# Kernel optimization log

Measured on AMD Instinct MI355X. Metric: run time of the kernel, lower is better.

## Reference

```python
import jax, jax.numpy as jnp
import numpy as np

C = 256        # branch_in_channels / head_conv
H, W = 160, 400
KPT_THR = 0.4  # forward_test default kpt_thr
ROOT_THR = 1.0 # self.root_thr
EPS = 1e-4


def _conv(x, w, b):
    # NCHW conv, SAME padding
    y = jax.lax.conv_general_dilated(x, w, (1, 1), 'SAME',
                                     dimension_numbers=('NCHW', 'OIHW', 'NCHW'))
    return y + b[None, :, None, None]


def _ctnet_head(x, w1, b1, w2, b2):
    # CtnetHead: Conv3x3 -> ReLU -> Conv1x1
    return _conv(jax.nn.relu(_conv(x, w1, b1)), w2, b2)


def setup_inputs() -> dict:
    key = jax.random.key(0)
    ks = jax.random.split(key, 16)
    s = 0.02
    def w3(k, co, ci):
        return jax.random.normal(k, (co, ci, 3, 3), jnp.float32) * s
    def w1k(k, co, ci):
        return jax.random.normal(k, (co, ci, 1, 1), jnp.float32) * s
    inp = {'f_hm': jax.random.normal(ks[0], (1, C, H, W), jnp.float32)}
    # four heads: centerpts (hm:1), keypts (hm:1), offset (2ch), reg (2ch)
    names = [('cpt', 1), ('kpt', 1), ('off', 2), ('reg', 2)]
    i = 1
    for name, cout in names:
        inp[f'{name}_w1'] = w3(ks[i], C, C); i += 1
        inp[f'{name}_b1'] = jnp.zeros((C,), jnp.float32)
        inp[f'{name}_w2'] = w1k(ks[i], cout, C); i += 1
        inp[f'{name}_b2'] = jnp.zeros((cout,), jnp.float32)
    return inp


def reference(f_hm, cpt_w1, cpt_b1, cpt_w2, cpt_b2,
              kpt_w1, kpt_b1, kpt_w2, kpt_b2,
              off_w1, off_b1, off_w2, off_b2,
              reg_w1, reg_b1, reg_w2, reg_b2):
    # heads
    hm = jnp.clip(jax.nn.sigmoid(_ctnet_head(f_hm, cpt_w1, cpt_b1, cpt_w2, cpt_b2)), EPS, 1.0 - EPS)
    kpts_hm = jnp.clip(jax.nn.sigmoid(_ctnet_head(f_hm, kpt_w1, kpt_b1, kpt_w2, kpt_b2)), EPS, 1.0 - EPS)
    pts_offset = _ctnet_head(f_hm, off_w1, off_b1, off_w2, off_b2)   # [1,2,H,W]
    int_offset = _ctnet_head(f_hm, reg_w1, reg_b1, reg_w2, reg_b2)   # [1,2,H,W]

    # ktdet_decode_fast: (1,3) max-pool NMS along width
    hmax = jax.lax.reduce_window(kpts_hm, -jnp.inf, jax.lax.max,
                                 (1, 1, 1, 3), (1, 1, 1, 1),
                                 ((0, 0), (0, 0), (0, 0), (1, 1)))
    heat_nms = kpts_hm * (hmax == kpts_hm).astype(kpts_hm.dtype)    # [1,1,H,W]

    # root-center mask: offset_y < root_thr AND heat_nms > kpt_thr, transposed to [W,H]
    mask_low = ((pts_offset[0, 1] < ROOT_THR) & (heat_nms[0, 0] > KPT_THR)).T  # [W,H] bool

    # coordinate maps: coord_mat channels are (x, y), permuted to [H,W,2]
    xs = jnp.arange(W, dtype=jnp.float32)
    ys = jnp.arange(H, dtype=jnp.float32)
    coord = jnp.stack(jnp.meshgrid(xs, ys, indexing='xy'), axis=-1)  # [H,W,2]

    offset_hw2 = jnp.transpose(pts_offset[0], (1, 2, 0))  # [H,W,2]
    error_hw2 = jnp.transpose(int_offset[0], (1, 2, 0))   # [H,W,2]
    root_mat = coord + offset_hw2
    align_mat = coord + error_hw2
    # heat_mat = heat_nms repeated to 2 channels; keypoint selection mask
    heat_hw = jnp.transpose(heat_nms[0], (1, 2, 0))        # [H,W,1]
    kpt_mask = jnp.tile(heat_hw, (1, 1, 2)) > KPT_THR      # [H,W,2] bool

    # host-side np.where / list extraction is excluded (data-dependent shapes);
    # all device-side math of ktdet_decode_fast is returned as fixed-shape arrays.
    return (hm, kpts_hm, pts_offset, int_offset, heat_nms,
            mask_low, root_mat, align_mat, kpt_mask)
```

## Files before the change

### kernel.cpp

```cpp
#include <hip/hip_runtime.h>

#define Hh 160
#define Ww 400
#define Cc 256
#define HW 64000
#define PITCH 401
#define XBASE 402
#define XT_PX 64963

typedef unsigned short u16;
typedef unsigned int   u32;
typedef __attribute__((ext_vector_type(8))) short short8;
typedef __attribute__((ext_vector_type(4))) float f32x4;

#define WA2_U16   (8*72*8*512)
#define XT_BYTES  ((size_t)8 * XT_PX * 64)
#define WS_NEED   ((size_t)WA2_U16 * 2 + XT_BYTES)

__device__ __forceinline__ u16 f2b(float v) {
    const u32 u = __float_as_uint(v);
    return (u16)((u + 0x7FFFu + ((u >> 16) & 1u)) >> 16);
}
__device__ __forceinline__ float sigclip(float v) {
    const float s = 1.0f / (1.0f + expf(-v));
    return fminf(fmaxf(s, 1e-4f), 1.0f - 1e-4f);
}
__device__ __forceinline__ void gload_lds16(const void* g, void* l) {
    __builtin_amdgcn_global_load_lds(
        (const __attribute__((address_space(1))) unsigned int*)g,
        (__attribute__((address_space(3))) unsigned int*)l, 16, 0, 0);
}

__global__ __launch_bounds__(256) void prep_weights(
    const float* __restrict__ w0, const float* __restrict__ w1p,
    const float* __restrict__ w2p, const float* __restrict__ w3p,
    u16* __restrict__ Wa2)
{
    const int blk  = blockIdx.x;
    const int head = blk / 72;
    const int s    = blk - head * 72;
    const int cib  = s / 9;
    const int tap  = s - cib * 9;
    const float* w = head == 0 ? w0 : head == 1 ? w1p : head == 2 ? w2p : w3p;

    const int t    = threadIdx.x;
    const int n16  = t & 15;
    const int mi   = (t >> 4) & 3;
    const int mblk = (t >> 6) & 1;
    const int mt   = t >> 7;
    const int m    = mt * 128 + mblk * 64 + mi * 16 + n16;
    const int hm   = head * 2 + mt;

    uint4* dst4 = (uint4*)Wa2 +
        ((size_t)((hm * 72 + s) * 2 + mblk) * 4 + mi) * 64 + n16;
    #pragma unroll
    for (int qq = 0; qq < 4; ++qq) {
        u16 tmp[8];
        #pragma unroll
        for (int j = 0; j < 8; ++j) {
            const int ci = cib * 32 + qq * 8 + j;
            tmp[j] = f2b(w[(size_t)m * (Cc * 9) + (size_t)ci * 9 + tap]);
        }
        dst4[qq * 16] = *(const uint4*)tmp;
    }
}

__global__ __launch_bounds__(256) void prep_x(
    const float* __restrict__ x, uint4* __restrict__ xt4)
{
    const int xx = blockIdx.x * 256 + threadIdx.x;
    const int y  = blockIdx.y;
    if (xx >= Ww) return;
    const int p  = y * Ww + xx;
    const size_t slot = (size_t)XBASE + (size_t)y * PITCH + xx;
    #pragma unroll
    for (int cib = 0; cib < 8; ++cib) {
        uint4* dst = xt4 + ((size_t)cib * XT_PX + slot) * 4;
        #pragma unroll
        for (int v = 0; v < 4; ++v) {
            u32 tmp[4];
            #pragma unroll
            for (int j = 0; j < 4; ++j) {
                const int ci = cib * 32 + v * 8 + j * 2;
                tmp[j] = (u32)f2b(x[(size_t)ci * HW + p])
                       | ((u32)f2b(x[(size_t)(ci + 1) * HW + p]) << 16);
            }
            dst[v] = *(const uint4*)tmp;
        }
    }
}

__global__ __launch_bounds__(64) void prep_zero(unsigned long long* __restrict__ xt64)
{
    const int b = blockIdx.x;
    int slot;
    if (b < 402)       slot = b;
    else if (b < 563)  slot = (b - 401) * PITCH;
    else               slot = 64561 + (b - 563);
    const int cib = threadIdx.x >> 3, j = threadIdx.x & 7;
    xt64[((size_t)cib * XT_PX + slot) * 8 + j] = 0ull;
}

__global__ __launch_bounds__(256, 2) void conv_mfma(
    const u16* __restrict__ Wa2, const u16* __restrict__ xt,
    const float* __restrict__ b1_0, const float* __restrict__ b1_1,
    const float* __restrict__ b1_2, const float* __restrict__ b1_3,
    const float* __restrict__ w2_0, const float* __restrict__ w2_1,
    const float* __restrict__ w2_2, const float* __restrict__ w2_3,
    const float* __restrict__ b2_0, const float* __restrict__ b2_1,
    const float* __restrict__ b2_2, const float* __restrict__ b2_3,
    float* __restrict__ out)
{
    __shared__ __align__(16) u16 Ab[2][8192];
    __shared__ __align__(16) u16 Bb[2][8448];
    __shared__ float Red[128][2][8];

    const int t    = threadIdx.x;
    const int lane = t & 63, wv = t >> 6;
    const int q    = lane >> 4, n16 = lane & 15;
    const int x0   = (blockIdx.x < 6) ? blockIdx.x * 64 : (Ww - 64);
    const int y0   = blockIdx.y * 2;
    const int head = blockIdx.z;
    const int nblk = wv & 1;
    const int mt   = wv >> 1;

    const u16* asrc0 = Wa2 + (size_t)(head * 2 + mt) * (72 * 4096)
                          + (size_t)(wv & 1) * 2048 + (size_t)lane * 8;
    const int u = lane >> 2;
    const int swz_main = ((lane & 3) ^ ((lane >> 3) & 3)) * 16 + u * 64;
    const int swz_tail = ((lane & 3) ^ ((1 + (lane >> 3)) & 3)) * 16 + (50 + u) * 64;
    const char* xtb = (const char*)xt;
    const size_t brow_slot = (size_t)(y0 - 1 + wv) * PITCH + (x0 - 1) + XBASE;

    int boff[4][3];
    #pragma unroll
    for (int nj = 0; nj < 4; ++nj)
        #pragma unroll
        for (int kx = 0; kx < 3; ++kx) {
            const int pxi = nj * 16 + n16 + kx;
            boff[nj][kx] = pxi * 64 + ((q ^ ((pxi >> 1) & 3)) * 16);
        }

    f32x4 acc[8][4];
    #pragma unroll
    for (int mi = 0; mi < 8; ++mi)
        #pragma unroll
        for (int nj = 0; nj < 4; ++nj) {
            f32x4 z = {0.f, 0.f, 0.f, 0.f};
            acc[mi][nj] = z;
        }

    {
        u16* adst = &Ab[0][wv * 2048];
        #pragma unroll
        for (int i = 0; i < 4; ++i)
            gload_lds16(asrc0 + i * 512, adst + i * 512);
        const char* src = xtb + brow_slot * 64;
        u16* bdst = &Bb[0][wv * 2112];
        #pragma unroll
        for (int i = 0; i < 4; ++i)
            gload_lds16(src + i * 1024 + swz_main, bdst + i * 512);
        gload_lds16(src + swz_tail, bdst + 1600);
    }
    __syncthreads();

    for (int cib = 0; cib < 8; ++cib) {
        const int cpar = cib & 1;
        #pragma unroll
        for (int tap = 0; tap < 9; ++tap) {
            const int par = cpar ^ (tap & 1);
            if (tap < 8 || cib < 7) {
                const int s_next = cib * 9 + tap + 1;
                const u16* src = asrc0 + (size_t)s_next * 4096;
                u16* adst = &Ab[par ^ 1][wv * 2048];
                #pragma unroll
                for (int i = 0; i < 4; ++i)
                    gload_lds16(src + i * 512, adst + i * 512);
            }
            if (tap == 4 && cib < 7) {
                const char* src = xtb + ((size_t)(cib + 1) * XT_PX + brow_slot) * 64;
                u16* bdst = &Bb[cpar ^ 1][wv * 2112];
                #pragma unroll
                for (int i = 0; i < 4; ++i)
                    gload_lds16(src + i * 1024 + swz_main, bdst + i * 512);
                gload_lds16(src + swz_tail, bdst + 1600);
            }
            const int ky = tap / 3, kx = tap - ky * 3;
            const u16*  abuf = &Ab[par][mt * 4096];
            const char* bbuf = (const char*)(&Bb[0][0]) + cpar * 16896
                             + (nblk + ky) * 4224;
            short8 b[4];
            #pragma unroll
            for (int nj = 0; nj < 4; ++nj)
                b[nj] = *(const short8*)(bbuf + boff[nj][kx]);
            #pragma unroll
            for (int mi = 0; mi < 8; ++mi) {
                const short8 a = *(const short8*)(abuf + mi * 512 + lane * 8);
                #pragma unroll
                for (int nj = 0; nj < 4; ++nj)
                    acc[mi][nj] = __builtin_amdgcn_mfma_f32_16x16x32_bf16(
                        a, b[nj], acc[mi][nj], 0, 0, 0);
            }
            __syncthreads();
        }
    }

    const float* b1 = head == 0 ? b1_0 : head == 1 ? b1_1 : head == 2 ? b1_2 : b1_3;
    const float* w2 = head == 0 ? w2_0 : head == 1 ? w2_1 : head == 2 ? w2_2 : w2_3;
    const float* b2 = head == 0 ? b2_0 : head == 1 ? b2_1 : head == 2 ? b2_2 : b2_3;
    const int cout   = (head < 2) ? 1 : 2;
    const int outoff = head == 0 ? 0 : head == 1 ? HW : head == 2 ? 2 * HW : 4 * HW;

    float p0[4] = {0.f, 0.f, 0.f, 0.f}, p1[4] = {0.f, 0.f, 0.f, 0.f};
    #pragma unroll
    for (int mi = 0; mi < 8; ++mi)
        #pragma unroll
        for (int r = 0; r < 4; ++r) {
            const int m = mt * 128 + mi * 16 + q * 4 + r;
            const float bb = b1[m], wc0 = w2[m];
            const float wc1 = (cout == 2) ? w2[Cc + m] : 0.0f;
            #pragma unroll
            for (int nj = 0; nj < 4; ++nj) {
                const float h = fmaxf(acc[mi][nj][r] + bb, 0.0f);
                p0[nj] = fmaf(wc0, h, p0[nj]);
                p1[nj] = fmaf(wc1, h, p1[nj]);
            }
        }

    #pragma unroll
    for (int nj = 0; nj < 4; ++nj) {
        const int n = nblk * 64 + nj * 16 + n16;
        Red[n][0][mt * 4 + q] = p0[nj];
        Red[n][1][mt * 4 + q] = p1[nj];
    }
    __syncthreads();

    if (t < cout * 128) {
        const int n = t & 127, c = t >> 7;
        float sv = b2[c];
        #pragma unroll
        for (int i = 0; i < 8; ++i) sv += Red[n][c][i];
        if (head < 2) sv = sigclip(sv);
        const int xg = x0 + (n & 63);
        const int yg = y0 + (n >> 6);
        out[outoff + c * HW + yg * Ww + xg] = sv;
    }
}

__global__ __launch_bounds__(256) void conv_head_simple(
    const float* __restrict__ x,
    const float* __restrict__ w1, const float* __restrict__ b1,
    const float* __restrict__ w2, const float* __restrict__ b2,
    float* __restrict__ out, int outoff, int cout, int apply_sig)
{
    const int px = threadIdx.x & 63;
    const int g  = threadIdx.x >> 6;
    const int x0 = blockIdx.x * 64;
    const int y  = blockIdx.y;
    const int xg = x0 + px;
    __shared__ float RedS[4][64][2];

    bool valid[9]; int xoff[9];
    #pragma unroll
    for (int dy = 0; dy < 3; ++dy) {
        const int yy = y + dy - 1;
        #pragma unroll
        for (int dx = 0; dx < 3; ++dx) {
            const int xx = xg + dx - 1;
            const int k = dy * 3 + dx;
            valid[k] = (yy >= 0 && yy < Hh && xx >= 0 && xx < Ww);
            xoff[k]  = valid[k] ? (yy * Ww + xx) : 0;
        }
    }
    float hid[64];
    #pragma unroll
    for (int mi = 0; mi < 64; ++mi) hid[mi] = b1[g * 64 + mi];
    for (int ci = 0; ci < Cc; ++ci) {
        const float* xch = x + (size_t)ci * HW;
        float xv[9];
        #pragma unroll
        for (int k = 0; k < 9; ++k) xv[k] = valid[k] ? xch[xoff[k]] : 0.0f;
        const float* wci = w1 + ((size_t)(g * 64) * Cc + ci) * 9;
        #pragma unroll 8
        for (int mi = 0; mi < 64; ++mi) {
            const float* wr = wci + (size_t)mi * (Cc * 9);
            float h = hid[mi];
            #pragma unroll
            for (int k = 0; k < 9; ++k) h = fmaf(wr[k], xv[k], h);
            hid[mi] = h;
        }
    }
    float p0 = 0.f, p1 = 0.f;
    #pragma unroll 8
    for (int mi = 0; mi < 64; ++mi) {
        const int m = g * 64 + mi;
        const float h = fmaxf(hid[mi], 0.0f);
        p0 = fmaf(w2[m], h, p0);
        if (cout == 2) p1 = fmaf(w2[Cc + m], h, p1);
    }
    RedS[g][px][0] = p0; RedS[g][px][1] = p1;
    __syncthreads();
    if (g == 0 && xg < Ww)
        for (int c = 0; c < cout; ++c) {
            float sv = b2[c] + RedS[0][px][c] + RedS[1][px][c]
                             + RedS[2][px][c] + RedS[3][px][c];
            if (apply_sig) sv = sigclip(sv);
            out[outoff + c * HW + y * Ww + xg] = sv;
        }
}

__global__ __launch_bounds__(256) void finalize_decode(float* __restrict__ out)
{
    const int i = blockIdx.x * 256 + threadIdx.x;
    if (i >= HW) return;
    const int h = i / Ww;
    const int w = i - h * Ww;

    const float k0 = out[HW + i];
    const float km = (w > 0)      ? out[HW + i - 1] : -1e30f;
    const float kp = (w < Ww - 1) ? out[HW + i + 1] : -1e30f;
    const float hmax = fmaxf(km, fmaxf(k0, kp));
    const float heat = (hmax == k0) ? k0 : 0.0f;

    const float off0 = out[2 * HW + i];
    const float off1 = out[3 * HW + i];
    const float reg0 = out[4 * HW + i];
    const float reg1 = out[5 * HW + i];
    const bool kmask = heat > 0.4f;

    out[6 * HW + i] = heat;
    out[7 * HW + w * Hh + h] = (off1 < 1.0f && kmask) ? 1.0f : 0.0f;
    out[8 * HW + 2 * i]      = (float)w + off0;
    out[8 * HW + 2 * i + 1]  = (float)h + off1;
    out[10 * HW + 2 * i]     = (float)w + reg0;
    out[10 * HW + 2 * i + 1] = (float)h + reg1;
    const float kb = kmask ? 1.0f : 0.0f;
    out[12 * HW + 2 * i]     = kb;
    out[12 * HW + 2 * i + 1] = kb;
}

extern "C" void kernel_launch(void* const* d_in, const int* in_sizes, int n_in,
                              void* d_out, int out_size, void* d_ws, size_t ws_size,
                              hipStream_t stream) {
    (void)in_sizes; (void)n_in; (void)out_size;
    const float* x = (const float*)d_in[0];
    float* out = (float*)d_out;

    if (ws_size >= WS_NEED) {
        u16* Wa2 = (u16*)d_ws;
        u16* xt  = Wa2 + WA2_U16;

        prep_weights<<<dim3(288), 256, 0, stream>>>(
            (const float*)d_in[1], (const float*)d_in[5],
            (const float*)d_in[9], (const float*)d_in[13], Wa2);
        prep_x<<<dim3(2, 160), 256, 0, stream>>>(x, (uint4*)xt);
        prep_zero<<<dim3(965), 64, 0, stream>>>((unsigned long long*)xt);

        conv_mfma<<<dim3(7, 80, 4), 256, 0, stream>>>(
            Wa2, xt,
            (const float*)d_in[2],  (const float*)d_in[6],
            (const float*)d_in[10], (const float*)d_in[14],
            (const float*)d_in[3],  (const float*)d_in[7],
            (const float*)d_in[11], (const float*)d_in[15],
            (const float*)d_in[4],  (const float*)d_in[8],
            (const float*)d_in[12], (const float*)d_in[16],
            out);
    } else {
        const int outoffs[4] = {0, HW, 2 * HW, 4 * HW};
        const int couts[4]   = {1, 1, 2, 2};
        for (int hd = 0; hd < 4; ++hd)
            conv_head_simple<<<dim3(7, 160), 256, 0, stream>>>(
                x,
                (const float*)d_in[1 + 4 * hd], (const float*)d_in[2 + 4 * hd],
                (const float*)d_in[3 + 4 * hd], (const float*)d_in[4 + 4 * hd],
                out, outoffs[hd], couts[hd], (hd < 2) ? 1 : 0);
    }
    finalize_decode<<<dim3(250), 256, 0, stream>>>(out);
}
```

Before: 471.1 us.

## Enlarge conv tile to 4 rows with 512 threads and triple-buffer weight loads

Doubles the block to 512 threads (8 waves) covering 4 output rows, so each weight tile loaded into LDS is reused across twice as many pixels. The A-weight pipeline becomes a 3-stage ring with fine-grained vmcnt waits and raw s_barrier in place of __syncthreads, and input loads are spread across taps. MFMA sections are wrapped in setprio, and the reduction buffer aliases the A buffer to save LDS. It aims to cut global weight traffic and barrier stalls, at the cost of more LDS per block and hand-counted waitcnt logic that is fragile.

```diff
diff --git a/kernel.cpp b/kernel.cpp
--- a/kernel.cpp
+++ b/kernel.cpp
@@ -15,6 +15,7 @@
 
 #define WA2_U16   (8*72*8*512)
 #define XT_BYTES  ((size_t)8 * XT_PX * 64)
+#define BSLICE    ((size_t)XT_PX * 64)
 #define WS_NEED   ((size_t)WA2_U16 * 2 + XT_BYTES)
 
 __device__ __forceinline__ u16 f2b(float v) {
@@ -101,7 +102,7 @@
     xt64[((size_t)cib * XT_PX + slot) * 8 + j] = 0ull;
 }
 
-__global__ __launch_bounds__(256, 2) void conv_mfma(
+__global__ __launch_bounds__(512, 2) void conv_mfma(
     const u16* __restrict__ Wa2, const u16* __restrict__ xt,
     const float* __restrict__ b1_0, const float* __restrict__ b1_1,
     const float* __restrict__ b1_2, const float* __restrict__ b1_3,
@@ -111,26 +112,40 @@
     const float* __restrict__ b2_2, const float* __restrict__ b2_3,
     float* __restrict__ out)
 {
-    __shared__ __align__(16) u16 Ab[2][8192];
-    __shared__ __align__(16) u16 Bb[2][8448];
-    __shared__ float Red[128][2][8];
+    __shared__ __align__(16) char SA[49152];
+    __shared__ __align__(16) u16 Bb[2][12672];
+
+    u16 (*Ab)[8192]   = (u16 (*)[8192])SA;
+    float (*Red)[2][8] = (float (*)[2][8])SA;
 
     const int t    = threadIdx.x;
     const int lane = t & 63, wv = t >> 6;
     const int q    = lane >> 4, n16 = lane & 15;
     const int x0   = (blockIdx.x < 6) ? blockIdx.x * 64 : (Ww - 64);
-    const int y0   = blockIdx.y * 2;
+    const int y0   = blockIdx.y * 4;
     const int head = blockIdx.z;
-    const int nblk = wv & 1;
-    const int mt   = wv >> 1;
-
+    const int r    = wv & 3;
+    const int mt   = wv >> 2;
+
+    const int adst_off = mt * 4096 + r * 1024;
     const u16* asrc0 = Wa2 + (size_t)(head * 2 + mt) * (72 * 4096)
-                          + (size_t)(wv & 1) * 2048 + (size_t)lane * 8;
-    const int u = lane >> 2;
-    const int swz_main = ((lane & 3) ^ ((lane >> 3) & 3)) * 16 + u * 64;
-    const int swz_tail = ((lane & 3) ^ ((1 + (lane >> 3)) & 3)) * 16 + (50 + u) * 64;
+                     + r * 1024 + lane * 8;
+
+    const long base_slot = (long)(y0 - 1) * PITCH + (x0 - 1) + XBASE;
+    int bsrc[4], dbo[4];
+    #pragma unroll
+    for (int j = 0; j < 4; ++j) {
+        const int db = wv * 3168 + (j < 3 ? j * 1024 : 2144);
+        dbo[j] = db;
+        const int d   = db + lane * 16;
+        const int row = d / 4224;
+        const int rem = d - row * 4224;
+        const int px  = rem >> 6;
+        const int qd  = (rem >> 4) & 3;
+        const int qs  = qd ^ ((px >> 1) & 3);
+        bsrc[j] = (int)((base_slot + row * PITCH + px) * 64 + qs * 16);
+    }
     const char* xtb = (const char*)xt;
-    const size_t brow_slot = (size_t)(y0 - 1 + wv) * PITCH + (x0 - 1) + XBASE;
 
     int boff[4][3];
     #pragma unroll
@@ -151,57 +166,69 @@
         }
 
     {
-        u16* adst = &Ab[0][wv * 2048];
-        #pragma unroll
-        for (int i = 0; i < 4; ++i)
-            gload_lds16(asrc0 + i * 512, adst + i * 512);
-        const char* src = xtb + brow_slot * 64;
-        u16* bdst = &Bb[0][wv * 2112];
-        #pragma unroll
-        for (int i = 0; i < 4; ++i)
-            gload_lds16(src + i * 1024 + swz_main, bdst + i * 512);
-        gload_lds16(src + swz_tail, bdst + 1600);
-    }
-    __syncthreads();
-
+        u16* d0 = Ab[0] + adst_off;
+        gload_lds16(asrc0,       d0);
+        gload_lds16(asrc0 + 512, d0 + 512);
+        #pragma unroll
+        for (int j = 0; j < 4; ++j)
+            gload_lds16(xtb + bsrc[j], (char*)(&Bb[0][0]) + dbo[j]);
+        u16* d1 = Ab[1] + adst_off;
+        gload_lds16(asrc0 + 4096,       d1);
+        gload_lds16(asrc0 + 4096 + 512, d1 + 512);
+    }
+    asm volatile("s_waitcnt vmcnt(2)" ::: "memory");
+    __builtin_amdgcn_s_barrier();
+    __builtin_amdgcn_sched_barrier(0);
+
+    int ap = 0;
     for (int cib = 0; cib < 8; ++cib) {
-        const int cpar = cib & 1;
+        const char* bread    = (const char*)(&Bb[cib & 1][0]);
+        char*       bwrite   = (char*)(&Bb[(cib & 1) ^ 1][0]);
+        const char* bsrc_cib = xtb + (size_t)(cib + 1) * BSLICE;
+        const bool  nl       = (cib < 7);
         #pragma unroll
         for (int tap = 0; tap < 9; ++tap) {
-            const int par = cpar ^ (tap & 1);
-            if (tap < 8 || cib < 7) {
-                const int s_next = cib * 9 + tap + 1;
-                const u16* src = asrc0 + (size_t)s_next * 4096;
-                u16* adst = &Ab[par ^ 1][wv * 2048];
-                #pragma unroll
-                for (int i = 0; i < 4; ++i)
-                    gload_lds16(src + i * 512, adst + i * 512);
-            }
-            if (tap == 4 && cib < 7) {
-                const char* src = xtb + ((size_t)(cib + 1) * XT_PX + brow_slot) * 64;
-                u16* bdst = &Bb[cpar ^ 1][wv * 2112];
-                #pragma unroll
-                for (int i = 0; i < 4; ++i)
-                    gload_lds16(src + i * 1024 + swz_main, bdst + i * 512);
-                gload_lds16(src + swz_tail, bdst + 1600);
+            const int s = cib * 9 + tap;
+            if (s < 70) {
+                const int aw = ap ? ap - 1 : 2;
+                const u16* src = asrc0 + (size_t)(s + 2) * 4096;
+                u16* dst = Ab[aw] + adst_off;
+                gload_lds16(src,       dst);
+                gload_lds16(src + 512, dst + 512);
+            }
+            if (nl && (tap == 0 || tap == 2 || tap == 4 || tap == 6)) {
+                const int j = tap >> 1;
+                gload_lds16(bsrc_cib + bsrc[j], bwrite + dbo[j]);
             }
             const int ky = tap / 3, kx = tap - ky * 3;
-            const u16*  abuf = &Ab[par][mt * 4096];
-            const char* bbuf = (const char*)(&Bb[0][0]) + cpar * 16896
-                             + (nblk + ky) * 4224;
-            short8 b[4];
+            const u16*  abuf = Ab[ap] + mt * 4096 + lane * 8;
+            const char* brow = bread + (r + ky) * 4224;
+            short8 bf[4];
             #pragma unroll
             for (int nj = 0; nj < 4; ++nj)
-                b[nj] = *(const short8*)(bbuf + boff[nj][kx]);
+                bf[nj] = *(const short8*)(brow + boff[nj][kx]);
+            __builtin_amdgcn_s_setprio(1);
             #pragma unroll
             for (int mi = 0; mi < 8; ++mi) {
-                const short8 a = *(const short8*)(abuf + mi * 512 + lane * 8);
+                const short8 a = *(const short8*)(abuf + mi * 512);
                 #pragma unroll
                 for (int nj = 0; nj < 4; ++nj)
                     acc[mi][nj] = __builtin_amdgcn_mfma_f32_16x16x32_bf16(
-                        a, b[nj], acc[mi][nj], 0, 0, 0);
-            }
-            __syncthreads();
+                        a, bf[nj], acc[mi][nj], 0, 0, 0);
+            }
+            __builtin_amdgcn_s_setprio(0);
+            __builtin_amdgcn_sched_barrier(0);
+            if (nl) {
+                if (tap == 8) asm volatile("s_waitcnt vmcnt(2)" ::: "memory");
+                else          asm volatile("s_waitcnt vmcnt(3)" ::: "memory");
+                __builtin_amdgcn_s_barrier();
+            } else {
+                if (tap < 7)       asm volatile("s_waitcnt vmcnt(2)" ::: "memory");
+                else if (tap == 7) asm volatile("s_waitcnt vmcnt(0)" ::: "memory");
+                if (tap < 8) __builtin_amdgcn_s_barrier();
+            }
+            __builtin_amdgcn_sched_barrier(0);
+            ap = (ap == 2) ? 0 : ap + 1;
         }
     }
 
@@ -215,28 +242,29 @@
     #pragma unroll
     for (int mi = 0; mi < 8; ++mi)
         #pragma unroll
-        for (int r = 0; r < 4; ++r) {
-            const int m = mt * 128 + mi * 16 + q * 4 + r;
+        for (int rr = 0; rr < 4; ++rr) {
+            const int m = mt * 128 + mi * 16 + q * 4 + rr;
             const float bb = b1[m], wc0 = w2[m];
             const float wc1 = (cout == 2) ? w2[Cc + m] : 0.0f;
             #pragma unroll
             for (int nj = 0; nj < 4; ++nj) {
-                const float h = fmaxf(acc[mi][nj][r] + bb, 0.0f);
+                const float h = fmaxf(acc[mi][nj][rr] + bb, 0.0f);
                 p0[nj] = fmaf(wc0, h, p0[nj]);
                 p1[nj] = fmaf(wc1, h, p1[nj]);
             }
         }
 
+    __syncthreads();
     #pragma unroll
     for (int nj = 0; nj < 4; ++nj) {
-        const int n = nblk * 64 + nj * 16 + n16;
+        const int n = r * 64 + nj * 16 + n16;
         Red[n][0][mt * 4 + q] = p0[nj];
         Red[n][1][mt * 4 + q] = p1[nj];
     }
     __syncthreads();
 
-    if (t < cout * 128) {
-        const int n = t & 127, c = t >> 7;
+    if (t < cout * 256) {
+        const int n = t & 255, c = t >> 8;
         float sv = b2[c];
         #pragma unroll
         for (int i = 0; i < 8; ++i) sv += Red[n][c][i];
@@ -356,7 +384,7 @@
         prep_x<<<dim3(2, 160), 256, 0, stream>>>(x, (uint4*)xt);
         prep_zero<<<dim3(965), 64, 0, stream>>>((unsigned long long*)xt);
 
-        conv_mfma<<<dim3(7, 80, 4), 256, 0, stream>>>(
+        conv_mfma<<<dim3(7, 40, 4), 512, 0, stream>>>(
             Wa2, xt,
             (const float*)d_in[2],  (const float*)d_in[6],
             (const float*)d_in[10], (const float*)d_in[14],
```

Result: slower. 492.5 us (+4.6%).
